# Optimization experiments

Measured on AMD Instinct MI355X. Metric: run time of the kernel, lower is better.

Reference implementation:

```python
import jax, jax.numpy as jnp
import numpy as np

V, D, NL, N, ED, K, DT = 32000, 256, 4, 16, 512, 4, 16  # dt_rank = ceil(256/16)
B, L = 2, 2048
EPS = 1e-5


def setup_inputs() -> dict:
    key = jax.random.key(0)
    ks = jax.random.split(key, 10)
    s = 0.02
    x = jax.random.randint(ks[0], (B, L), 0, V)
    embed_t = jax.random.normal(ks[1], (V, D)) * s
    rms_w = jnp.ones((NL, D))
    in_proj_w = jax.random.normal(ks[2], (NL, 2 * ED, D)) * s
    conv_w = jax.random.normal(ks[3], (NL, ED, K)) * 0.1
    conv_b = jnp.zeros((NL, ED))
    x_proj_w = jax.random.normal(ks[4], (NL, DT + 2 * N, ED)) * s
    dt_proj_w = jax.random.normal(ks[5], (NL, ED, DT)) * (DT ** -0.5)
    dt_proj_b = jax.random.uniform(ks[6], (NL, ED), minval=-4.0, maxval=-2.0)  # softplus -> small dt
    A_log = jnp.log(jnp.tile(jnp.arange(1, N + 1, dtype=jnp.float32), (NL, ED, 1)))  # S4D-real init
    D_p = jnp.ones((NL, ED))
    out_proj_w = jax.random.normal(ks[7], (NL, D, ED)) * s
    norm_w = jnp.ones(D)
    norm_b = jnp.zeros(D)
    head_w = jax.random.normal(ks[8], (V, D)) * s
    head_b = jnp.zeros(V)
    return dict(x=x, embed_t=embed_t, rms_w=rms_w, in_proj_w=in_proj_w, conv_w=conv_w,
                conv_b=conv_b, x_proj_w=x_proj_w, dt_proj_w=dt_proj_w, dt_proj_b=dt_proj_b,
                A_log=A_log, D_p=D_p, out_proj_w=out_proj_w, norm_w=norm_w, norm_b=norm_b,
                head_w=head_w, head_b=head_b)


def _rmsnorm(x, w):
    return x * jax.lax.rsqrt(jnp.mean(x * x, axis=-1, keepdims=True) + EPS) * w


def _layernorm(x, w, b):
    mu = jnp.mean(x, axis=-1, keepdims=True)
    var = jnp.mean((x - mu) ** 2, axis=-1, keepdims=True)
    return (x - mu) * jax.lax.rsqrt(var + EPS) * w + b


def _scan_combine(left, right):
    al, bl = left
    ar, br = right
    return (al * ar, ar * bl + br)


def _mamba_block(h, rw, ipw, cw, cb, xpw, dpw, dpb, alog, dp, opw):
    # h: (B, L, D). Residual block: h + mixer(rmsnorm(h))
    xin = _rmsnorm(h, rw)
    xz = xin @ ipw.T                      # (B, L, 2*ED)
    xc, z = jnp.split(xz, 2, axis=-1)
    # causal depthwise conv1d, kernel K, left-pad K-1 (== torch padding=K-1 then [:L])
    k = cw.shape[1]
    seqlen = xc.shape[1]
    xp = jnp.pad(xc, ((0, 0), (k - 1, 0), (0, 0)))
    xc = sum(xp[:, i:i + seqlen, :] * cw[:, i] for i in range(k)) + cb
    xc = jax.nn.silu(xc)
    # selective SSM
    dt_rank = dpw.shape[1]
    n = alog.shape[1]
    dbc = xc @ xpw.T                      # (B, L, dt_rank + 2N)
    delta, Bm, Cm = jnp.split(dbc, [dt_rank, dt_rank + n], axis=-1)
    delta = jax.nn.softplus(delta @ dpw.T + dpb)   # (B, L, ED)
    A = -jnp.exp(alog)                              # (ED, N)
    dA = jnp.exp(delta[..., None] * A)              # (B, L, ED, N)
    dBx = (delta[..., None] * Bm[:, :, None, :]) * xc[..., None]  # (B, L, ED, N)
    _, hs = jax.lax.associative_scan(_scan_combine, (dA, dBx), axis=1)  # h_t = dA_t*h_{t-1} + dBx_t
    y = jnp.einsum('blen,bln->ble', hs, Cm) + dp * xc
    y = y * jax.nn.silu(z)
    return h + y @ opw.T


def reference(x, embed_t, rms_w, in_proj_w, conv_w, conv_b, x_proj_w, dt_proj_w,
              dt_proj_b, A_log, D_p, out_proj_w, norm_w, norm_b, head_w, head_b):
    h = embed_t[x]                        # (B, L, D)
    for i in range(rms_w.shape[0]):
        h = _mamba_block(h, rms_w[i], in_proj_w[i], conv_w[i], conv_b[i], x_proj_w[i],
                         dt_proj_w[i], dt_proj_b[i], A_log[i], D_p[i], out_proj_w[i])
    hn = _layernorm(h, norm_w, norm_b)
    return hn @ head_w.T + head_b         # (B, L, V)
```

## Files before the change

kernel.cpp:

```cpp
#include <hip/hip_runtime.h>
#include <hip/hip_bf16.h>
#include <math.h>

#define Bq   2
#define Lq   2048
#define Dq   256
#define NLq  4
#define Nst  16
#define EDq  512
#define Kq   4
#define DTq  16
#define Vq   32000
#define Rq   (Bq*Lq)
#define NCv  64
#define LCv  (Lq/NCv)
#define RPB  4

typedef __attribute__((ext_vector_type(8))) __bf16 bf16x8v;
typedef __attribute__((ext_vector_type(4))) float f32x4v;
typedef __attribute__((address_space(1))) const void GV;
typedef __attribute__((address_space(3))) void LV;

__device__ __forceinline__ unsigned short to_bf16(float f) {
    unsigned int u = __float_as_uint(f);
    unsigned int r = (u + 0x7FFFu + ((u >> 16) & 1u)) >> 16;
    return (unsigned short)r;
}
__device__ __forceinline__ float from_bf16(unsigned short u) {
    return __uint_as_float(((unsigned int)u) << 16);
}

__global__ __launch_bounds__(256) void convert_bf16(const float* __restrict__ in,
                                                    unsigned short* __restrict__ out, int n) {
    int i = (blockIdx.x * 256 + threadIdx.x) * 4;
    if (i + 3 < n) {
        float4 v = *(const float4*)&in[i];
        ushort4 o;
        o.x = to_bf16(v.x); o.y = to_bf16(v.y); o.z = to_bf16(v.z); o.w = to_bf16(v.w);
        *(ushort4*)&out[i] = o;
    }
}

__global__ __launch_bounds__(256) void embed_kernel(const int* __restrict__ x,
                                                    const float* __restrict__ et,
                                                    float* __restrict__ h) {
    int r = blockIdx.x;
    int d = threadIdx.x;
    h[r * Dq + d] = et[x[r] * Dq + d];
}

__global__ __launch_bounds__(256) void rmsnorm_kernel(const float* __restrict__ h,
                                                      const float* __restrict__ w,
                                                      unsigned short* __restrict__ out) {
    int r = blockIdx.x;
    int d = threadIdx.x;
    float v = h[r * Dq + d];
    float ss = v * v;
#pragma unroll
    for (int o = 32; o > 0; o >>= 1) ss += __shfl_down(ss, o);
    __shared__ float sb[4];
    if ((threadIdx.x & 63) == 0) sb[threadIdx.x >> 6] = ss;
    __syncthreads();
    float tot = sb[0] + sb[1] + sb[2] + sb[3];
    float scale = rsqrtf(tot * (1.0f / Dq) + 1e-5f);
    out[r * Dq + d] = to_bf16(v * scale * w[d]);
}

__global__ __launch_bounds__(256) void layernorm_kernel(const float* __restrict__ h,
                                                        const float* __restrict__ w,
                                                        const float* __restrict__ b,
                                                        unsigned short* __restrict__ out) {
    int r = blockIdx.x;
    int d = threadIdx.x;
    float v = h[r * Dq + d];
    float s = v, s2 = v * v;
#pragma unroll
    for (int o = 32; o > 0; o >>= 1) { s += __shfl_down(s, o); s2 += __shfl_down(s2, o); }
    __shared__ float sb[8];
    if ((threadIdx.x & 63) == 0) { sb[threadIdx.x >> 6] = s; sb[4 + (threadIdx.x >> 6)] = s2; }
    __syncthreads();
    float S  = sb[0] + sb[1] + sb[2] + sb[3];
    float S2 = sb[4] + sb[5] + sb[6] + sb[7];
    float mu = S * (1.0f / Dq);
    float var = S2 * (1.0f / Dq) - mu * mu;
    out[r * Dq + d] = to_bf16((v - mu) * rsqrtf(var + 1e-5f) * w[d] + b[d]);
}

template<int BM, int BN, typename OT, bool ACC>
__global__ __launch_bounds__(256) void gemm_mfma(const unsigned short* __restrict__ A,
                                                 const unsigned short* __restrict__ W,
                                                 const float* __restrict__ bias,
                                                 OT* __restrict__ C,
                                                 int M, int N, int K) {
    constexpr int WGM = (BM == 128 && BN == 64) ? 4 : 2;
    constexpr int WGN = 4 / WGM;
    constexpr int MR = BM / (WGM * 16);
    constexpr int NR = BN / (WGN * 16);
    constexpr int AR = BM / 64;
    constexpr int BR = BN / 64;
    __shared__ unsigned short As[BM * 32];
    __shared__ unsigned short Bs[BN * 32];

    const int gx = gridDim.x;
    const int nwg = gx * gridDim.y;
    int flat = blockIdx.y * gx + blockIdx.x;
    if ((nwg & 7) == 0) {
        int cpx = nwg >> 3;
        flat = (flat & 7) * cpx + (flat >> 3);
    }
    const int m0 = (flat / gx) * BM, n0 = (flat % gx) * BN;

    const int tid = threadIdx.x;
    const int wid = tid >> 6, lane = tid & 63;
    const int wrow = (wid / WGN) * (BM / WGM);
    const int wcol = (wid % WGN) * (BN / WGN);

    f32x4v acc[MR][NR];
#pragma unroll
    for (int i = 0; i < MR; i++)
#pragma unroll
        for (int j = 0; j < NR; j++) acc[i][j] = (f32x4v){0.f, 0.f, 0.f, 0.f};

    const int srow = lane >> 2;
    const int skoff = (lane & 3) * 8;
    const unsigned short* gA = A + (size_t)(m0 + wid * (16 * AR) + srow) * K + skoff;
    unsigned short* lA = As + wid * (512 * AR) + lane * 8;
    const unsigned short* gW = W + (size_t)(n0 + wid * (16 * BR) + srow) * K + skoff;
    unsigned short* lB = Bs + wid * (512 * BR) + lane * 8;

    const int l15 = lane & 15, lk = (lane >> 4) * 8;

    for (int kt = 0; kt < K; kt += 32) {
        __syncthreads();
#pragma unroll
        for (int p = 0; p < AR; p++)
            __builtin_amdgcn_global_load_lds((GV*)(gA + kt + (size_t)p * 16 * K),
                                             (LV*)(lA + p * 512), 16, 0, 0);
#pragma unroll
        for (int p = 0; p < BR; p++)
            __builtin_amdgcn_global_load_lds((GV*)(gW + kt + (size_t)p * 16 * K),
                                             (LV*)(lB + p * 512), 16, 0, 0);
        __syncthreads();

        bf16x8v a[MR], b[NR];
#pragma unroll
        for (int i = 0; i < MR; i++)
            a[i] = *(const bf16x8v*)&As[(wrow + i * 16 + l15) * 32 + lk];
#pragma unroll
        for (int j = 0; j < NR; j++)
            b[j] = *(const bf16x8v*)&Bs[(wcol + j * 16 + l15) * 32 + lk];
#pragma unroll
        for (int i = 0; i < MR; i++)
#pragma unroll
            for (int j = 0; j < NR; j++)
                acc[i][j] = __builtin_amdgcn_mfma_f32_16x16x32_bf16(a[i], b[j], acc[i][j], 0, 0, 0);
    }

    const int rbase = m0 + wrow + (lane >> 4) * 4;
    const int cbase = n0 + wcol + l15;
#pragma unroll
    for (int i = 0; i < MR; i++) {
#pragma unroll
        for (int j = 0; j < NR; j++) {
            int col = cbase + j * 16;
            float bv = bias ? bias[col] : 0.f;
#pragma unroll
            for (int r = 0; r < 4; r++) {
                int row = rbase + i * 16 + r;
                float v = acc[i][j][r] + bv;
                OT* dst = &C[(size_t)row * N + col];
                if constexpr (ACC) { *dst = v + *dst; }
                else if constexpr (__is_same(OT, unsigned short)) { *dst = to_bf16(v); }
                else { *dst = v; }
            }
        }
    }
}

__global__ __launch_bounds__(256) void mid_fused(const unsigned short* __restrict__ xz,
                                                 const float* __restrict__ cw,
                                                 const float* __restrict__ cb,
                                                 const unsigned short* __restrict__ xpw16,
                                                 const float* __restrict__ dtw,
                                                 const float* __restrict__ dtb,
                                                 unsigned short* __restrict__ xc,
                                                 float* __restrict__ dbc,
                                                 unsigned short* __restrict__ dlt) {
    const int r0 = blockIdx.x * RPB;
    const int l0 = r0 & (Lq - 1);
    const int tid = threadIdx.x;
    __shared__ float xcs[RPB][EDq];
    __shared__ float dbs[RPB][16];

#pragma unroll
    for (int ch = 0; ch < 2; ch++) {
        const int e = tid + ch * 256;
        const float4 wv = *(const float4*)&cw[e * 4];
        const float bb = cb[e];
        float x0 = 0.f, x1 = 0.f, x2 = 0.f;
        if (l0 > 0) {
            x0 = from_bf16(xz[(size_t)(r0 - 3) * 1024 + e]);
            x1 = from_bf16(xz[(size_t)(r0 - 2) * 1024 + e]);
            x2 = from_bf16(xz[(size_t)(r0 - 1) * 1024 + e]);
        }
#pragma unroll
        for (int t = 0; t < RPB; t++) {
            float x3 = from_bf16(xz[(size_t)(r0 + t) * 1024 + e]);
            float a = bb;
            a = fmaf(x0, wv.x, a);
            a = fmaf(x1, wv.y, a);
            a = fmaf(x2, wv.z, a);
            a = fmaf(x3, wv.w, a);
            float s = a / (1.0f + __expf(-a));
            xcs[t][e] = s;
            xc[(size_t)(r0 + t) * EDq + e] = to_bf16(s);
            x0 = x1; x1 = x2; x2 = x3;
        }
    }
    __syncthreads();

    const int j = tid >> 2, sub = tid & 3;
    const unsigned short* wr = &xpw16[j * EDq + sub * 128];
#pragma unroll
    for (int t = 0; t < RPB; t++) {
        float part = 0.f;
        if (j < 48) {
            const float* xr = &xcs[t][sub * 128];
            for (int k = 0; k < 128; k += 4) {
                ushort4 wv = *(const ushort4*)&wr[k];
                float4 xv = *(const float4*)&xr[k];
                part = fmaf(from_bf16(wv.x), xv.x, part);
                part = fmaf(from_bf16(wv.y), xv.y, part);
                part = fmaf(from_bf16(wv.z), xv.z, part);
                part = fmaf(from_bf16(wv.w), xv.w, part);
            }
        }
        part += __shfl_xor(part, 1);
        part += __shfl_xor(part, 2);
        if (j < 48 && sub == 0) {
            dbc[(size_t)(r0 + t) * 48 + j] = part;
            if (j < 16) dbs[t][j] = part;
        }
    }
    __syncthreads();

#pragma unroll
    for (int ch = 0; ch < 2; ch++) {
        const int e = tid + ch * 256;
        float wrg[16];
#pragma unroll
        for (int g = 0; g < 4; g++) {
            float4 v = *(const float4*)&dtw[e * 16 + g * 4];
            wrg[g * 4] = v.x; wrg[g * 4 + 1] = v.y; wrg[g * 4 + 2] = v.z; wrg[g * 4 + 3] = v.w;
        }
        const float bb = dtb[e];
#pragma unroll
        for (int t = 0; t < RPB; t++) {
            float a = bb;
#pragma unroll
            for (int k = 0; k < 16; k++) a = fmaf(dbs[t][k], wrg[k], a);
            float sp = (a > 20.f) ? a : log1pf(__expf(a));
            dlt[(size_t)(r0 + t) * EDq + e] = to_bf16(sp);
        }
    }
}

__global__ __launch_bounds__(256) void scan_pass1(const unsigned short* __restrict__ dlt,
                                                  const unsigned short* __restrict__ xc,
                                                  const float* __restrict__ dbc,
                                                  const float* __restrict__ A_log,
                                                  float* __restrict__ cA,
                                                  float* __restrict__ cB) {
    int gid = blockIdx.x * 256 + threadIdx.x;
    int sub = gid & 3;
    int e = (gid >> 2) & (EDq - 1);
    int bc = gid >> 11;
    int rbase = bc * LCv;

    float Aa[4];
#pragma unroll
    for (int k = 0; k < 4; k++) Aa[k] = -__expf(A_log[e * 16 + sub * 4 + k]);
    float pA[4] = {1.f, 1.f, 1.f, 1.f};
    float hB[4] = {0.f, 0.f, 0.f, 0.f};

#pragma unroll 4
    for (int t = 0; t < LCv; t++) {
        int r = rbase + t;
        float d = from_bf16(dlt[(size_t)r * EDq + e]);
        float xv = from_bf16(xc[(size_t)r * EDq + e]);
        float dx = d * xv;
        float4 Bm = *(const float4*)&dbc[(size_t)r * 48 + 16 + sub * 4];
        float Bk[4] = {Bm.x, Bm.y, Bm.z, Bm.w};
#pragma unroll
        for (int k = 0; k < 4; k++) {
            float dA = __expf(d * Aa[k]);
            hB[k] = fmaf(dA, hB[k], dx * Bk[k]);
            pA[k] *= dA;
        }
    }
    size_t ob = ((size_t)bc * EDq + e) * 16 + sub * 4;
    *(float4*)&cA[ob] = make_float4(pA[0], pA[1], pA[2], pA[3]);
    *(float4*)&cB[ob] = make_float4(hB[0], hB[1], hB[2], hB[3]);
}

__global__ __launch_bounds__(256) void scan_combine(const float* __restrict__ cA,
                                                    const float* __restrict__ cB,
                                                    float* __restrict__ cP) {
    int idx = blockIdx.x * 256 + threadIdx.x;
    int en = idx & 8191;
    int b = idx >> 13;
    float hc = 0.f;
    for (int c = 0; c < NCv; c++) {
        size_t base = ((size_t)(b * NCv + c) << 13) + en;
        cP[base] = hc;
        hc = fmaf(cA[base], hc, cB[base]);
    }
}

__global__ __launch_bounds__(256) void scan_pass2(const unsigned short* __restrict__ dlt,
                                                  const unsigned short* __restrict__ xc,
                                                  const float* __restrict__ dbc,
                                                  const float* __restrict__ A_log,
                                                  const float* __restrict__ cP,
                                                  const float* __restrict__ Dp,
                                                  const unsigned short* __restrict__ xz,
                                                  unsigned short* __restrict__ y) {
    int gid = blockIdx.x * 256 + threadIdx.x;
    int sub = gid & 3;
    int e = (gid >> 2) & (EDq - 1);
    int bc = gid >> 11;
    int rbase = bc * LCv;

    float Aa[4];
#pragma unroll
    for (int k = 0; k < 4; k++) Aa[k] = -__expf(A_log[e * 16 + sub * 4 + k]);
    float hh[4];
    size_t pb = ((size_t)bc * EDq + e) * 16 + sub * 4;
    {
        float4 v = *(const float4*)&cP[pb];
        hh[0] = v.x; hh[1] = v.y; hh[2] = v.z; hh[3] = v.w;
    }
    const float Dv = Dp[e];

#pragma unroll 4
    for (int t = 0; t < LCv; t++) {
        int r = rbase + t;
        float d = from_bf16(dlt[(size_t)r * EDq + e]);
        float xv = from_bf16(xc[(size_t)r * EDq + e]);
        float dx = d * xv;
        float4 Bm = *(const float4*)&dbc[(size_t)r * 48 + 16 + sub * 4];
        float4 Cm = *(const float4*)&dbc[(size_t)r * 48 + 32 + sub * 4];
        float Bk[4] = {Bm.x, Bm.y, Bm.z, Bm.w};
        float Ck[4] = {Cm.x, Cm.y, Cm.z, Cm.w};
        float cacc = 0.f;
#pragma unroll
        for (int k = 0; k < 4; k++) {
            float dA = __expf(d * Aa[k]);
            hh[k] = fmaf(dA, hh[k], dx * Bk[k]);
            cacc = fmaf(hh[k], Ck[k], cacc);
        }
        cacc += __shfl_xor(cacc, 1);
        cacc += __shfl_xor(cacc, 2);
        if (sub == 0) {
            float yv = fmaf(Dv, xv, cacc);
            float zv = from_bf16(xz[(size_t)r * 1024 + EDq + e]);
            float sz = zv / (1.0f + __expf(-zv));
            y[(size_t)r * EDq + e] = to_bf16(yv * sz);
        }
    }
}

extern "C" void kernel_launch(void* const* d_in, const int* in_sizes, int n_in,
                              void* d_out, int out_size, void* d_ws, size_t ws_size,
                              hipStream_t stream) {
    const int*   x         = (const int*)d_in[0];
    const float* embed_t   = (const float*)d_in[1];
    const float* rms_w     = (const float*)d_in[2];
    const float* in_proj_w = (const float*)d_in[3];
    const float* conv_w    = (const float*)d_in[4];
    const float* conv_b    = (const float*)d_in[5];
    const float* x_proj_w  = (const float*)d_in[6];
    const float* dt_proj_w = (const float*)d_in[7];
    const float* dt_proj_b = (const float*)d_in[8];
    const float* A_log     = (const float*)d_in[9];
    const float* D_p       = (const float*)d_in[10];
    const float* out_proj_w= (const float*)d_in[11];
    const float* norm_w    = (const float*)d_in[12];
    const float* norm_b    = (const float*)d_in[13];
    const float* head_w    = (const float*)d_in[14];
    const float* head_b    = (const float*)d_in[15];
    float* out = (float*)d_out;

    const size_t CSZ = (size_t)Bq * NCv * EDq * Nst;

    float* ws = (float*)d_ws;
    float* h    = ws;
    float* dbc  = h   + (size_t)Rq * Dq;
    float* cA   = dbc + (size_t)Rq * 48;
    float* cB   = cA  + CSZ;
    float* cP   = cB  + CSZ;
    float* fend = cP  + CSZ;

    unsigned short* xz16  = (unsigned short*)fend;
    unsigned short* xc16  = xz16  + (size_t)Rq * 1024;
    unsigned short* dlt16 = xc16  + (size_t)Rq * EDq;
    unsigned short* xin16 = dlt16 + (size_t)Rq * EDq;
    unsigned short* yb16  = xin16 + (size_t)Rq * Dq;
    unsigned short* hn16  = yb16  + (size_t)Rq * EDq;
    unsigned short* w16i  = hn16  + (size_t)Rq * Dq;
    unsigned short* w16o  = w16i  + (size_t)NLq * 1024 * Dq;
    unsigned short* w16xp = w16o  + (size_t)NLq * Dq * EDq;
    unsigned short* w16h  = w16xp + (size_t)NLq * 48 * EDq;

    convert_bf16<<<(NLq * 1024 * Dq) / 1024, 256, 0, stream>>>(in_proj_w, w16i, NLq * 1024 * Dq);
    convert_bf16<<<(NLq * Dq * EDq) / 1024, 256, 0, stream>>>(out_proj_w, w16o, NLq * Dq * EDq);
    convert_bf16<<<(NLq * 48 * EDq) / 1024, 256, 0, stream>>>(x_proj_w, w16xp, NLq * 48 * EDq);
    convert_bf16<<<(Vq * Dq) / 1024, 256, 0, stream>>>(head_w, w16h, Vq * Dq);

    embed_kernel<<<Rq, 256, 0, stream>>>(x, embed_t, h);

    for (int i = 0; i < NLq; i++) {
        rmsnorm_kernel<<<Rq, 256, 0, stream>>>(h, rms_w + i * Dq, xin16);
        gemm_mfma<128, 128, unsigned short, false><<<dim3(1024 / 128, Rq / 128), 256, 0, stream>>>(
            xin16, w16i + (size_t)i * 1024 * Dq, nullptr, xz16, Rq, 1024, Dq);
        mid_fused<<<Rq / RPB, 256, 0, stream>>>(
            xz16, conv_w + i * EDq * Kq, conv_b + i * EDq,
            w16xp + (size_t)i * 48 * EDq,
            dt_proj_w + (size_t)i * EDq * DTq, dt_proj_b + i * EDq,
            xc16, dbc, dlt16);
        scan_pass1<<<(Bq * NCv * EDq * 4) / 256, 256, 0, stream>>>(
            dlt16, xc16, dbc, A_log + i * EDq * Nst, cA, cB);
        scan_combine<<<(Bq * EDq * Nst) / 256, 256, 0, stream>>>(cA, cB, cP);
        scan_pass2<<<(Bq * NCv * EDq * 4) / 256, 256, 0, stream>>>(
            dlt16, xc16, dbc, A_log + i * EDq * Nst, cP, D_p + i * EDq, xz16, yb16);
        gemm_mfma<64, 64, float, true><<<dim3(Dq / 64, Rq / 64), 256, 0, stream>>>(
            yb16, w16o + (size_t)i * Dq * EDq, nullptr, h, Rq, Dq, EDq);
    }

    layernorm_kernel<<<Rq, 256, 0, stream>>>(h, norm_w, norm_b, hn16);
    gemm_mfma<128, 128, float, false><<<dim3(Vq / 128, Rq / 128), 256, 0, stream>>>(
        hn16, w16h, head_b, out, Rq, Vq, Dq);
}
```

Measured before the change: 621.3 us.

## Fuse conv/proj and three scan stages into one cooperative kernel with grid syncs

Replaces the four per-layer kernels (mid_fused, scan_pass1, scan_combine, scan_pass2) with a single cooperative kernel that runs each stage in turn, separated by grid.sync(). This removes three kernel launches and the launch gaps between them in each layer. The grid is 1024 blocks of 256 threads, so it only runs if all blocks fit at once. Grid-wide barriers cost something, and the combine stage uses only 64 blocks while the rest sit idle. The GEMM epilogue also gains a bf16 accumulate path, which is not used here.

```diff
diff --git a/kernel.cpp b/kernel.cpp
--- a/kernel.cpp
+++ b/kernel.cpp
@@ -1,6 +1,9 @@
 #include <hip/hip_runtime.h>
 #include <hip/hip_bf16.h>
+#include <hip/hip_cooperative_groups.h>
 #include <math.h>
+
+namespace cg = cooperative_groups;
 
 #define Bq   2
 #define Lq   2048
@@ -169,203 +172,202 @@
                 int row = rbase + i * 16 + r;
                 float v = acc[i][j][r] + bv;
                 OT* dst = &C[(size_t)row * N + col];
-                if constexpr (ACC) { *dst = v + *dst; }
-                else if constexpr (__is_same(OT, unsigned short)) { *dst = to_bf16(v); }
-                else { *dst = v; }
-            }
-        }
-    }
-}
-
-__global__ __launch_bounds__(256) void mid_fused(const unsigned short* __restrict__ xz,
-                                                 const float* __restrict__ cw,
-                                                 const float* __restrict__ cb,
-                                                 const unsigned short* __restrict__ xpw16,
-                                                 const float* __restrict__ dtw,
-                                                 const float* __restrict__ dtb,
-                                                 unsigned short* __restrict__ xc,
-                                                 float* __restrict__ dbc,
-                                                 unsigned short* __restrict__ dlt) {
-    const int r0 = blockIdx.x * RPB;
-    const int l0 = r0 & (Lq - 1);
+                if constexpr (__is_same(OT, unsigned short)) {
+                    if constexpr (ACC) *dst = to_bf16(v + from_bf16(*dst));
+                    else               *dst = to_bf16(v);
+                } else {
+                    if constexpr (ACC) *dst = v + *dst;
+                    else               *dst = v;
+                }
+            }
+        }
+    }
+}
+
+__global__ __launch_bounds__(256, 4) void layer_middle_coop(
+        const unsigned short* __restrict__ xz,
+        const float* __restrict__ cw, const float* __restrict__ cb,
+        const unsigned short* __restrict__ xpw16,
+        const float* __restrict__ dtw, const float* __restrict__ dtb,
+        const float* __restrict__ A_log, const float* __restrict__ Dp,
+        unsigned short* __restrict__ xc, float* __restrict__ dbc,
+        unsigned short* __restrict__ dlt,
+        float* __restrict__ cA, float* __restrict__ cB, float* __restrict__ cP,
+        unsigned short* __restrict__ y) {
+    cg::grid_group grid = cg::this_grid();
     const int tid = threadIdx.x;
-    __shared__ float xcs[RPB][EDq];
-    __shared__ float dbs[RPB][16];
-
-#pragma unroll
-    for (int ch = 0; ch < 2; ch++) {
-        const int e = tid + ch * 256;
-        const float4 wv = *(const float4*)&cw[e * 4];
-        const float bb = cb[e];
-        float x0 = 0.f, x1 = 0.f, x2 = 0.f;
-        if (l0 > 0) {
-            x0 = from_bf16(xz[(size_t)(r0 - 3) * 1024 + e]);
-            x1 = from_bf16(xz[(size_t)(r0 - 2) * 1024 + e]);
-            x2 = from_bf16(xz[(size_t)(r0 - 1) * 1024 + e]);
-        }
+    const int bid = blockIdx.x;
+
+    {
+        const int r0 = bid * RPB;
+        const int l0 = r0 & (Lq - 1);
+        __shared__ float xcs[RPB][EDq];
+        __shared__ float dbs[RPB][16];
+
+#pragma unroll
+        for (int ch = 0; ch < 2; ch++) {
+            const int e = tid + ch * 256;
+            const float4 wv = *(const float4*)&cw[e * 4];
+            const float bb = cb[e];
+            float x0 = 0.f, x1 = 0.f, x2 = 0.f;
+            if (l0 > 0) {
+                x0 = from_bf16(xz[(size_t)(r0 - 3) * 1024 + e]);
+                x1 = from_bf16(xz[(size_t)(r0 - 2) * 1024 + e]);
+                x2 = from_bf16(xz[(size_t)(r0 - 1) * 1024 + e]);
+            }
+#pragma unroll
+            for (int t = 0; t < RPB; t++) {
+                float x3 = from_bf16(xz[(size_t)(r0 + t) * 1024 + e]);
+                float a = bb;
+                a = fmaf(x0, wv.x, a);
+                a = fmaf(x1, wv.y, a);
+                a = fmaf(x2, wv.z, a);
+                a = fmaf(x3, wv.w, a);
+                float s = a / (1.0f + __expf(-a));
+                xcs[t][e] = s;
+                xc[(size_t)(r0 + t) * EDq + e] = to_bf16(s);
+                x0 = x1; x1 = x2; x2 = x3;
+            }
+        }
+        __syncthreads();
+
+        const int j = tid >> 2, sub = tid & 3;
+        const unsigned short* wr = &xpw16[j * EDq + sub * 128];
 #pragma unroll
         for (int t = 0; t < RPB; t++) {
-            float x3 = from_bf16(xz[(size_t)(r0 + t) * 1024 + e]);
-            float a = bb;
-            a = fmaf(x0, wv.x, a);
-            a = fmaf(x1, wv.y, a);
-            a = fmaf(x2, wv.z, a);
-            a = fmaf(x3, wv.w, a);
-            float s = a / (1.0f + __expf(-a));
-            xcs[t][e] = s;
-            xc[(size_t)(r0 + t) * EDq + e] = to_bf16(s);
-            x0 = x1; x1 = x2; x2 = x3;
-        }
-    }
-    __syncthreads();
-
-    const int j = tid >> 2, sub = tid & 3;
-    const unsigned short* wr = &xpw16[j * EDq + sub * 128];
-#pragma unroll
-    for (int t = 0; t < RPB; t++) {
-        float part = 0.f;
-        if (j < 48) {
-            const float* xr = &xcs[t][sub * 128];
-            for (int k = 0; k < 128; k += 4) {
-                ushort4 wv = *(const ushort4*)&wr[k];
-                float4 xv = *(const float4*)&xr[k];
-                part = fmaf(from_bf16(wv.x), xv.x, part);
-                part = fmaf(from_bf16(wv.y), xv.y, part);
-                part = fmaf(from_bf16(wv.z), xv.z, part);
-                part = fmaf(from_bf16(wv.w), xv.w, part);
-            }
-        }
-        part += __shfl_xor(part, 1);
-        part += __shfl_xor(part, 2);
-        if (j < 48 && sub == 0) {
-            dbc[(size_t)(r0 + t) * 48 + j] = part;
-            if (j < 16) dbs[t][j] = part;
-        }
-    }
-    __syncthreads();
-
-#pragma unroll
-    for (int ch = 0; ch < 2; ch++) {
-        const int e = tid + ch * 256;
-        float wrg[16];
-#pragma unroll
-        for (int g = 0; g < 4; g++) {
-            float4 v = *(const float4*)&dtw[e * 16 + g * 4];
-            wrg[g * 4] = v.x; wrg[g * 4 + 1] = v.y; wrg[g * 4 + 2] = v.z; wrg[g * 4 + 3] = v.w;
-        }
-        const float bb = dtb[e];
-#pragma unroll
-        for (int t = 0; t < RPB; t++) {
-            float a = bb;
-#pragma unroll
-            for (int k = 0; k < 16; k++) a = fmaf(dbs[t][k], wrg[k], a);
-            float sp = (a > 20.f) ? a : log1pf(__expf(a));
-            dlt[(size_t)(r0 + t) * EDq + e] = to_bf16(sp);
-        }
-    }
-}
-
-__global__ __launch_bounds__(256) void scan_pass1(const unsigned short* __restrict__ dlt,
-                                                  const unsigned short* __restrict__ xc,
-                                                  const float* __restrict__ dbc,
-                                                  const float* __restrict__ A_log,
-                                                  float* __restrict__ cA,
-                                                  float* __restrict__ cB) {
-    int gid = blockIdx.x * 256 + threadIdx.x;
-    int sub = gid & 3;
-    int e = (gid >> 2) & (EDq - 1);
-    int bc = gid >> 11;
-    int rbase = bc * LCv;
-
-    float Aa[4];
-#pragma unroll
-    for (int k = 0; k < 4; k++) Aa[k] = -__expf(A_log[e * 16 + sub * 4 + k]);
-    float pA[4] = {1.f, 1.f, 1.f, 1.f};
-    float hB[4] = {0.f, 0.f, 0.f, 0.f};
+            float part = 0.f;
+            if (j < 48) {
+                const float* xr = &xcs[t][sub * 128];
+                for (int k = 0; k < 128; k += 4) {
+                    ushort4 wv = *(const ushort4*)&wr[k];
+                    float4 xv = *(const float4*)&xr[k];
+                    part = fmaf(from_bf16(wv.x), xv.x, part);
+                    part = fmaf(from_bf16(wv.y), xv.y, part);
+                    part = fmaf(from_bf16(wv.z), xv.z, part);
+                    part = fmaf(from_bf16(wv.w), xv.w, part);
+                }
+            }
+            part += __shfl_xor(part, 1);
+            part += __shfl_xor(part, 2);
+            if (j < 48 && sub == 0) {
+                dbc[(size_t)(r0 + t) * 48 + j] = part;
+                if (j < 16) dbs[t][j] = part;
+            }
+        }
+        __syncthreads();
+
+#pragma unroll
+        for (int ch = 0; ch < 2; ch++) {
+            const int e = tid + ch * 256;
+            float wrg[16];
+#pragma unroll
+            for (int g = 0; g < 4; g++) {
+                float4 v = *(const float4*)&dtw[e * 16 + g * 4];
+                wrg[g * 4] = v.x; wrg[g * 4 + 1] = v.y; wrg[g * 4 + 2] = v.z; wrg[g * 4 + 3] = v.w;
+            }
+            const float bb = dtb[e];
+#pragma unroll
+            for (int t = 0; t < RPB; t++) {
+                float a = bb;
+#pragma unroll
+                for (int k = 0; k < 16; k++) a = fmaf(dbs[t][k], wrg[k], a);
+                float sp = (a > 20.f) ? a : log1pf(__expf(a));
+                dlt[(size_t)(r0 + t) * EDq + e] = to_bf16(sp);
+            }
+        }
+    }
+    grid.sync();
+
+    {
+        int gid = bid * 256 + tid;
+        int sub = gid & 3;
+        int e = (gid >> 2) & (EDq - 1);
+        int bc = gid >> 11;
+        int rbase = bc * LCv;
+
+        float Aa[4];
+#pragma unroll
+        for (int k = 0; k < 4; k++) Aa[k] = -__expf(A_log[e * 16 + sub * 4 + k]);
+        float pA[4] = {1.f, 1.f, 1.f, 1.f};
+        float hB[4] = {0.f, 0.f, 0.f, 0.f};
 
 #pragma unroll 4
-    for (int t = 0; t < LCv; t++) {
-        int r = rbase + t;
-        float d = from_bf16(dlt[(size_t)r * EDq + e]);
-        float xv = from_bf16(xc[(size_t)r * EDq + e]);
-        float dx = d * xv;
-        float4 Bm = *(const float4*)&dbc[(size_t)r * 48 + 16 + sub * 4];
-        float Bk[4] = {Bm.x, Bm.y, Bm.z, Bm.w};
-#pragma unroll
-        for (int k = 0; k < 4; k++) {
-            float dA = __expf(d * Aa[k]);
-            hB[k] = fmaf(dA, hB[k], dx * Bk[k]);
-            pA[k] *= dA;
-        }
-    }
-    size_t ob = ((size_t)bc * EDq + e) * 16 + sub * 4;
-    *(float4*)&cA[ob] = make_float4(pA[0], pA[1], pA[2], pA[3]);
-    *(float4*)&cB[ob] = make_float4(hB[0], hB[1], hB[2], hB[3]);
-}
-
-__global__ __launch_bounds__(256) void scan_combine(const float* __restrict__ cA,
-                                                    const float* __restrict__ cB,
-                                                    float* __restrict__ cP) {
-    int idx = blockIdx.x * 256 + threadIdx.x;
-    int en = idx & 8191;
-    int b = idx >> 13;
-    float hc = 0.f;
-    for (int c = 0; c < NCv; c++) {
-        size_t base = ((size_t)(b * NCv + c) << 13) + en;
-        cP[base] = hc;
-        hc = fmaf(cA[base], hc, cB[base]);
-    }
-}
-
-__global__ __launch_bounds__(256) void scan_pass2(const unsigned short* __restrict__ dlt,
-                                                  const unsigned short* __restrict__ xc,
-                                                  const float* __restrict__ dbc,
-                                                  const float* __restrict__ A_log,
-                                                  const float* __restrict__ cP,
-                                                  const float* __restrict__ Dp,
-                                                  const unsigned short* __restrict__ xz,
-                                                  unsigned short* __restrict__ y) {
-    int gid = blockIdx.x * 256 + threadIdx.x;
-    int sub = gid & 3;
-    int e = (gid >> 2) & (EDq - 1);
-    int bc = gid >> 11;
-    int rbase = bc * LCv;
-
-    float Aa[4];
-#pragma unroll
-    for (int k = 0; k < 4; k++) Aa[k] = -__expf(A_log[e * 16 + sub * 4 + k]);
-    float hh[4];
-    size_t pb = ((size_t)bc * EDq + e) * 16 + sub * 4;
+        for (int t = 0; t < LCv; t++) {
+            int r = rbase + t;
+            float d = from_bf16(dlt[(size_t)r * EDq + e]);
+            float xv = from_bf16(xc[(size_t)r * EDq + e]);
+            float dx = d * xv;
+            float4 Bm = *(const float4*)&dbc[(size_t)r * 48 + 16 + sub * 4];
+            float Bk[4] = {Bm.x, Bm.y, Bm.z, Bm.w};
+#pragma unroll
+            for (int k = 0; k < 4; k++) {
+                float dA = __expf(d * Aa[k]);
+                hB[k] = fmaf(dA, hB[k], dx * Bk[k]);
+                pA[k] *= dA;
+            }
+        }
+        size_t ob = ((size_t)bc * EDq + e) * 16 + sub * 4;
+        *(float4*)&cA[ob] = make_float4(pA[0], pA[1], pA[2], pA[3]);
+        *(float4*)&cB[ob] = make_float4(hB[0], hB[1], hB[2], hB[3]);
+    }
+    grid.sync();
+
+    if (bid < 64) {
+        int idx = bid * 256 + tid;
+        int en = idx & 8191;
+        int b = idx >> 13;
+        float hc = 0.f;
+        for (int c = 0; c < NCv; c++) {
+            size_t base = ((size_t)(b * NCv + c) << 13) + en;
+            cP[base] = hc;
+            hc = fmaf(cA[base], hc, cB[base]);
+        }
+    }
+    grid.sync();
+
     {
-        float4 v = *(const float4*)&cP[pb];
-        hh[0] = v.x; hh[1] = v.y; hh[2] = v.z; hh[3] = v.w;
-    }
-    const float Dv = Dp[e];
+        int gid = bid * 256 + tid;
+        int sub = gid & 3;
+        int e = (gid >> 2) & (EDq - 1);
+        int bc = gid >> 11;
+        int rbase = bc * LCv;
+
+        float Aa[4];
+#pragma unroll
+        for (int k = 0; k < 4; k++) Aa[k] = -__expf(A_log[e * 16 + sub * 4 + k]);
+        float hh[4];
+        size_t pb = ((size_t)bc * EDq + e) * 16 + sub * 4;
+        {
+            float4 v = *(const float4*)&cP[pb];
+            hh[0] = v.x; hh[1] = v.y; hh[2] = v.z; hh[3] = v.w;
+        }
+        const float Dv = Dp[e];
 
 #pragma unroll 4
-    for (int t = 0; t < LCv; t++) {
-        int r = rbase + t;
-        float d = from_bf16(dlt[(size_t)r * EDq + e]);
-        float xv = from_bf16(xc[(size_t)r * EDq + e]);
-        float dx = d * xv;
-        float4 Bm = *(const float4*)&dbc[(size_t)r * 48 + 16 + sub * 4];
-        float4 Cm = *(const float4*)&dbc[(size_t)r * 48 + 32 + sub * 4];
-        float Bk[4] = {Bm.x, Bm.y, Bm.z, Bm.w};
-        float Ck[4] = {Cm.x, Cm.y, Cm.z, Cm.w};
-        float cacc = 0.f;
-#pragma unroll
-        for (int k = 0; k < 4; k++) {
-            float dA = __expf(d * Aa[k]);
-            hh[k] = fmaf(dA, hh[k], dx * Bk[k]);
-            cacc = fmaf(hh[k], Ck[k], cacc);
-        }
-        cacc += __shfl_xor(cacc, 1);
-        cacc += __shfl_xor(cacc, 2);
-        if (sub == 0) {
-            float yv = fmaf(Dv, xv, cacc);
-            float zv = from_bf16(xz[(size_t)r * 1024 + EDq + e]);
-            float sz = zv / (1.0f + __expf(-zv));
-            y[(size_t)r * EDq + e] = to_bf16(yv * sz);
+        for (int t = 0; t < LCv; t++) {
+            int r = rbase + t;
+            float d = from_bf16(dlt[(size_t)r * EDq + e]);
+            float xv = from_bf16(xc[(size_t)r * EDq + e]);
+            float dx = d * xv;
+            float4 Bm = *(const float4*)&dbc[(size_t)r * 48 + 16 + sub * 4];
+            float4 Cm = *(const float4*)&dbc[(size_t)r * 48 + 32 + sub * 4];
+            float Bk[4] = {Bm.x, Bm.y, Bm.z, Bm.w};
+            float Ck[4] = {Cm.x, Cm.y, Cm.z, Cm.w};
+            float cacc = 0.f;
+#pragma unroll
+            for (int k = 0; k < 4; k++) {
+                float dA = __expf(d * Aa[k]);
+                hh[k] = fmaf(dA, hh[k], dx * Bk[k]);
+                cacc = fmaf(hh[k], Ck[k], cacc);
+            }
+            cacc += __shfl_xor(cacc, 1);
+            cacc += __shfl_xor(cacc, 2);
+            if (sub == 0) {
+                float yv = fmaf(Dv, xv, cacc);
+                float zv = from_bf16(xz[(size_t)r * 1024 + EDq + e]);
+                float sz = zv / (1.0f + __expf(-zv));
+                y[(size_t)r * EDq + e] = to_bf16(yv * sz);
+            }
         }
     }
 }
@@ -421,18 +423,30 @@
 
     for (int i = 0; i < NLq; i++) {
         rmsnorm_kernel<<<Rq, 256, 0, stream>>>(h, rms_w + i * Dq, xin16);
-        gemm_mfma<128, 128, unsigned short, false><<<dim3(1024 / 128, Rq / 128), 256, 0, stream>>>(
+        gemm_mfma<128, 128, unsigned short, false>
+            <<<dim3(1024 / 128, Rq / 128), 256, 0, stream>>>(
             xin16, w16i + (size_t)i * 1024 * Dq, nullptr, xz16, Rq, 1024, Dq);
-        mid_fused<<<Rq / RPB, 256, 0, stream>>>(
-            xz16, conv_w + i * EDq * Kq, conv_b + i * EDq,
-            w16xp + (size_t)i * 48 * EDq,
-            dt_proj_w + (size_t)i * EDq * DTq, dt_proj_b + i * EDq,
-            xc16, dbc, dlt16);
-        scan_pass1<<<(Bq * NCv * EDq * 4) / 256, 256, 0, stream>>>(
-            dlt16, xc16, dbc, A_log + i * EDq * Nst, cA, cB);
-        scan_combine<<<(Bq * EDq * Nst) / 256, 256, 0, stream>>>(cA, cB, cP);
-        scan_pass2<<<(Bq * NCv * EDq * 4) / 256, 256, 0, stream>>>(
-            dlt16, xc16, dbc, A_log + i * EDq * Nst, cP, D_p + i * EDq, xz16, yb16);
+
+        const unsigned short* cxz = xz16;
+        const float* ccw  = conv_w + i * EDq * Kq;
+        const float* ccb  = conv_b + i * EDq;
+        const unsigned short* cxp = w16xp + (size_t)i * 48 * EDq;
+        const float* cdtw = dt_proj_w + (size_t)i * EDq * DTq;
+        const float* cdtb = dt_proj_b + i * EDq;
+        const float* cal  = A_log + i * EDq * Nst;
+        const float* cdp  = D_p + i * EDq;
+        unsigned short* cxc = xc16;
+        float* cdbc = dbc;
+        unsigned short* cdlt = dlt16;
+        float *ca = cA, *cb = cB, *cp = cP;
+        unsigned short* cy = yb16;
+        void* args[] = {(void*)&cxz, (void*)&ccw, (void*)&ccb, (void*)&cxp,
+                        (void*)&cdtw, (void*)&cdtb, (void*)&cal, (void*)&cdp,
+                        (void*)&cxc, (void*)&cdbc, (void*)&cdlt,
+                        (void*)&ca, (void*)&cb, (void*)&cp, (void*)&cy};
+        hipLaunchCooperativeKernel((const void*)layer_middle_coop,
+                                   dim3(Rq / RPB), dim3(256), args, 0, stream);
+
         gemm_mfma<64, 64, float, true><<<dim3(Dq / 64, Rq / 64), 256, 0, stream>>>(
             yb16, w16o + (size_t)i * Dq * EDq, nullptr, h, Rq, Dq, EDq);
     }
```

New measurement: 1.885 ms. +203.5%, slower.
